# Kernel tuning notes

Hardware: AMD Instinct MI355X
Metric: run time of the kernel (lower is better)

## Reference

```python
import jax, jax.numpy as jnp
import numpy as np

NMS_RADIUS = 2.0   # cfgs.NMS_radius (meters)
EPS = 1e-6         # torch nn.PairwiseDistance default eps (added to the diff)
M = 16384          # number of keypoint candidates
SCENE = 100.0      # scene extent in meters


def setup_inputs() -> dict:
    key = jax.random.key(0)
    k1, k2 = jax.random.split(key)
    nodes = jax.random.uniform(k1, (M, 3), dtype=jnp.float32) * SCENE
    overlap_score = jax.random.normal(k2, (M,), dtype=jnp.float32)
    return {"nodes": nodes, "overlap_score": overlap_score}


def _greedy_nms(nodes, radius):
    """Sequential greedy NMS: keep node i iff its distance to every
    already-kept node exceeds radius. Faithful to the torch loop:
    (dis > radius).sum() == n_kept  <=>  all kept dists > radius."""
    n = nodes.shape[0]

    def body(i, mask):
        # torch nn.PairwiseDistance computes ||x1 - x2 + eps||_2
        d = jnp.linalg.norm(nodes[i] - nodes + EPS, axis=-1)  # [n]
        keep = jnp.all(jnp.where(mask, d > radius, True))
        return mask.at[i].set(keep)

    mask0 = jnp.zeros(n, dtype=bool).at[0].set(True)
    return jax.lax.fori_loop(1, n, body, mask0)


def reference(nodes, overlap_score):
    # sort by overlap score descending, run greedy NMS, unsort the mask
    order = jnp.argsort(-overlap_score)
    mask_sorted = _greedy_nms(nodes[order], NMS_RADIUS)
    mask = jnp.zeros_like(mask_sorted).at[order].set(mask_sorted)
    nms_length = mask.sum(dtype=jnp.int32)[None]
    return mask, nms_length
```

## Files before the change

kernel.cpp:

```cpp
#include <hip/hip_runtime.h>


#define M_PTS    16384
#define RADIUS   2.0f
#define EPS_D    1e-6f
#define GRID_N   25
#define NCELLS   (GRID_N * GRID_N * GRID_N)
#define CELL_CAP 12
#define K_NBR    12
#define ACT_CAP  4608


__device__ __forceinline__ int cell_of(float v) {
  int c = (int)(v * 0.25f);
  return c < 0 ? 0 : (c > GRID_N - 1 ? GRID_N - 1 : c);
}

__global__ __launch_bounds__(256) void zero_kernel(int4* __restrict__ p) {
  int i = blockIdx.x * 256 + threadIdx.x;
  if (i < 8003) p[i] = make_int4(0, 0, 0, 0);
}

__global__ __launch_bounds__(256) void grid_build(
    const float* __restrict__ nodes, const float* __restrict__ score,
    float4* __restrict__ pts, int* __restrict__ cell_cnt,
    unsigned short* __restrict__ cell_list) {
  int i = blockIdx.x * 256 + threadIdx.x;
  if (i >= M_PTS) return;
  float4 p;
  p.x = nodes[3 * i + 0];
  p.y = nodes[3 * i + 1];
  p.z = nodes[3 * i + 2];
  p.w = score[i];
  pts[i] = p;
  int cid = (cell_of(p.x) * GRID_N + cell_of(p.y)) * GRID_N + cell_of(p.z);
  int pos = atomicAdd(&cell_cnt[cid], 1);
  if (pos < CELL_CAP) cell_list[cid * CELL_CAP + pos] = (unsigned short)i;
}

__global__ __launch_bounds__(256) void nbr_scan(
    const float4* __restrict__ pts, const int* __restrict__ cell_cnt,
    const unsigned short* __restrict__ cell_list,
    int* __restrict__ cnt, unsigned short* __restrict__ nbr) {
  int t = blockIdx.x * 256 + threadIdx.x;
  int i = t / 27;
  int d = t - i * 27;
  if (i >= M_PTS) return;
  const float4 pi = pts[i];
  int cx = cell_of(pi.x) + (d / 9) - 1;
  int cy = cell_of(pi.y) + ((d / 3) % 3) - 1;
  int cz = cell_of(pi.z) + (d % 3) - 1;
  if (cx < 0 || cx >= GRID_N || cy < 0 || cy >= GRID_N ||
      cz < 0 || cz >= GRID_N) return;
  int cid = (cx * GRID_N + cy) * GRID_N + cz;
  int m = cell_cnt[cid];
  if (m > CELL_CAP) m = CELL_CAP;
  for (int s = 0; s < m; ++s) {
    int j = cell_list[cid * CELL_CAP + s];
    float4 pj = pts[j];
    bool earlier = (pj.w > pi.w) || ((pj.w == pi.w) && (j < i));
    if (!earlier) continue;
    float ddx = __fadd_rn(__fsub_rn(pi.x, pj.x), EPS_D);
    float ddy = __fadd_rn(__fsub_rn(pi.y, pj.y), EPS_D);
    float ddz = __fadd_rn(__fsub_rn(pi.z, pj.z), EPS_D);
    float d2 = __fadd_rn(__fadd_rn(__fmul_rn(ddx, ddx), __fmul_rn(ddy, ddy)),
                         __fmul_rn(ddz, ddz));
    float dist = __fsqrt_rn(d2);
    if (!(dist > RADIUS)) {
      int pos = atomicAdd(&cnt[i], 1);
      if (pos < K_NBR) nbr[i * K_NBR + pos] = (unsigned short)j;
    }
  }
}

__global__ __launch_bounds__(1024) void solve_kernel(
    const int* __restrict__ cnt, const unsigned short* __restrict__ nbr,
    int* __restrict__ out, int out_size) {
  __shared__ unsigned char mask_[M_PTS];
  __shared__ unsigned int nbr_s[ACT_CAP][6];
  __shared__ unsigned int act[ACT_CAP];
  __shared__ int act_n, total;
  volatile unsigned char* mask = mask_;

  const int tid = threadIdx.x;
  if (tid == 0) { act_n = 0; total = 0; }
  __syncthreads();

  for (int k = tid; k < M_PTS; k += 1024) {
    mask_[k] = 1;
    int c = cnt[k];
    if (c > K_NBR) c = K_NBR;
    if (c > 0) {
      int pos = atomicAdd(&act_n, 1);
      if (pos < ACT_CAP) act[pos] = (unsigned)k | ((unsigned)c << 16);
    }
  }
  __syncthreads();
  const int na_raw = act_n;
  const bool ok = (na_raw <= ACT_CAP);
  const int na = ok ? na_raw : ACT_CAP;

  if (ok) {
    for (int a = tid; a < na; a += 1024) {
      int k = (int)(act[a] & 0xFFFFu);
      const unsigned int* src = (const unsigned int*)(nbr + (size_t)k * K_NBR);
#pragma unroll
      for (int w = 0; w < 6; ++w) nbr_s[a][w] = src[w];
    }
  }
  __syncthreads();

  if (ok) {
    for (int grp = 0; grp < 128; ++grp) {
      for (int g = 0; g < 4; ++g) {
        for (int a = tid; a < na; a += 1024) {
          unsigned e = act[a];
          int k = (int)(e & 0xFFFFu);
          int c = (int)(e >> 16);
          const unsigned short* row = (const unsigned short*)nbr_s[a];
          int kp = 1;
          for (int t = 0; t < c; ++t) kp &= (int)(mask[row[t]] ^ 1);
          if (kp != (int)mask[k]) mask[k] = (unsigned char)kp;
        }
        asm volatile("" ::: "memory");
      }
      int any = 0;
      for (int a = tid; a < na; a += 1024) {
        unsigned e = act[a];
        int k = (int)(e & 0xFFFFu);
        int c = (int)(e >> 16);
        const unsigned short* row = (const unsigned short*)nbr_s[a];
        int kp = 1;
        for (int t = 0; t < c; ++t) kp &= (int)(mask[row[t]] ^ 1);
        if (kp != (int)mask[k]) { mask[k] = (unsigned char)kp; any = 1; }
      }
      if (__syncthreads_count(any) == 0) break;
    }
  } else {
    __shared__ int changed;
    for (int it = 0; it < 512; ++it) {
      if (tid == 0) changed = 0;
      __syncthreads();
      int any = 0;
      for (int k = tid; k < M_PTS; k += 1024) {
        int c = cnt[k]; if (c > K_NBR) c = K_NBR;
        if (!c) continue;
        int kp = 1;
        for (int t = 0; t < c; ++t) kp &= (int)(mask[nbr[k * K_NBR + t]] ^ 1);
        if (kp != (int)mask[k]) { mask_[k] = (unsigned char)kp; any = 1; }
      }
      if (any) changed = 1;
      __syncthreads();
      if (!changed) break;
    }
  }
  __syncthreads();

  int ks = 0;
  for (int k = tid; k < M_PTS; k += 1024) {
    int m = (int)mask_[k];
    out[k] = m;
    ks += m;
  }
#pragma unroll
  for (int off = 32; off > 0; off >>= 1) ks += __shfl_down(ks, off, 64);
  if ((tid & 63) == 0) atomicAdd(&total, ks);
  __syncthreads();
  if (tid == 0) out[out_size - 1] = total;
}

extern "C" void kernel_launch(void* const* d_in, const int* in_sizes, int n_in,
                              void* d_out, int out_size, void* d_ws, size_t ws_size,
                              hipStream_t stream) {
  const float* nodes = (const float*)d_in[0];
  const float* score = (const float*)d_in[1];
  int* out = (int*)d_out;

  char* ws = (char*)d_ws;
  float4* pts = (float4*)ws;
  int* cell_cnt = (int*)(ws + 262144);
  int* cnt = (int*)(ws + 324644);
  unsigned short* cell_list = (unsigned short*)(ws + 393216);
  unsigned short* nbr = (unsigned short*)(ws + 770048);

  zero_kernel<<<32, 256, 0, stream>>>((int4*)(ws + 262144));
  grid_build<<<64, 256, 0, stream>>>(nodes, score, pts, cell_cnt, cell_list);
  nbr_scan<<<1728, 256, 0, stream>>>(pts, cell_cnt, cell_list, cnt, nbr);
  solve_kernel<<<1, 1024, 0, stream>>>(cnt, nbr, out, out_size);
}
```

Baseline: 40.88 us.

## Keep active-point neighbor lists in registers and aggregate compaction atomics per wavefront

The solve kernel drops the shared-memory neighbor table. Each thread now holds up to five active entries, with their first three neighbor indices cached in registers, and falls back to global memory for longer lists. Compaction of active points uses one ballot-based atomic per wavefront instead of one per thread. The relaxation loop no longer runs four unsynchronized sweeps per check; it syncs after every sweep and is capped at 96 iterations, which may need more barriers and may stop before convergence if more passes are needed.

```diff
diff --git a/kernel.cpp b/kernel.cpp
--- a/kernel.cpp
+++ b/kernel.cpp
@@ -8,7 +8,8 @@
 #define NCELLS   (GRID_N * GRID_N * GRID_N)
 #define CELL_CAP 12
 #define K_NBR    12
-#define ACT_CAP  4608
+#define EPT      5
+#define ACT_PAD  (EPT * 1024)
 
 
 __device__ __forceinline__ int cell_of(float v) {
@@ -77,61 +78,68 @@
     const int* __restrict__ cnt, const unsigned short* __restrict__ nbr,
     int* __restrict__ out, int out_size) {
   __shared__ unsigned char mask_[M_PTS];
-  __shared__ unsigned int nbr_s[ACT_CAP][6];
-  __shared__ unsigned int act[ACT_CAP];
+  __shared__ unsigned int act[ACT_PAD];
   __shared__ int act_n, total;
   volatile unsigned char* mask = mask_;
 
   const int tid = threadIdx.x;
+  const int lane = tid & 63;
   if (tid == 0) { act_n = 0; total = 0; }
+  for (int a = tid; a < ACT_PAD; a += 1024) act[a] = 0u;
   __syncthreads();
 
   for (int k = tid; k < M_PTS; k += 1024) {
     mask_[k] = 1;
     int c = cnt[k];
     if (c > K_NBR) c = K_NBR;
+    unsigned long long b = __ballot(c > 0);
+    int wcnt = __popcll(b);
+    int wbase = 0;
+    if (lane == 0 && wcnt) wbase = atomicAdd(&act_n, wcnt);
+    wbase = __shfl(wbase, 0, 64);
     if (c > 0) {
-      int pos = atomicAdd(&act_n, 1);
-      if (pos < ACT_CAP) act[pos] = (unsigned)k | ((unsigned)c << 16);
+      int pos = wbase + __popcll(b & ((1ull << lane) - 1ull));
+      if (pos < ACT_PAD) act[pos] = (unsigned)k | ((unsigned)c << 16);
     }
   }
   __syncthreads();
-  const int na_raw = act_n;
-  const bool ok = (na_raw <= ACT_CAP);
-  const int na = ok ? na_raw : ACT_CAP;
+  const int na = act_n;
+  const bool ok = (na <= ACT_PAD);
 
-  if (ok) {
-    for (int a = tid; a < na; a += 1024) {
-      int k = (int)(act[a] & 0xFFFFu);
-      const unsigned int* src = (const unsigned int*)(nbr + (size_t)k * K_NBR);
+  unsigned ae[EPT];
+  unsigned short r0[EPT], r1[EPT], r2[EPT];
 #pragma unroll
-      for (int w = 0; w < 6; ++w) nbr_s[a][w] = src[w];
-    }
+  for (int e = 0; e < EPT; ++e) {
+    unsigned v = act[tid + e * 1024];
+    ae[e] = v;
+    int k = (int)(v & 0xFFFFu);
+    int c = (int)(v >> 16);
+    const unsigned short* row = nbr + (size_t)k * K_NBR;
+    r0[e] = (c > 0) ? row[0] : (unsigned short)0;
+    r1[e] = (c > 1) ? row[1] : (unsigned short)0;
+    r2[e] = (c > 2) ? row[2] : (unsigned short)0;
   }
   __syncthreads();
 
   if (ok) {
-    for (int grp = 0; grp < 128; ++grp) {
-      for (int g = 0; g < 4; ++g) {
-        for (int a = tid; a < na; a += 1024) {
-          unsigned e = act[a];
-          int k = (int)(e & 0xFFFFu);
-          int c = (int)(e >> 16);
-          const unsigned short* row = (const unsigned short*)nbr_s[a];
-          int kp = 1;
-          for (int t = 0; t < c; ++t) kp &= (int)(mask[row[t]] ^ 1);
-          if (kp != (int)mask[k]) mask[k] = (unsigned char)kp;
+    for (int it = 0; it < 96; ++it) {
+      int any = 0;
+      int m0[EPT];
+#pragma unroll
+      for (int e = 0; e < EPT; ++e) m0[e] = (int)mask[r0[e]];
+#pragma unroll
+      for (int e = 0; e < EPT; ++e) {
+        unsigned v = ae[e];
+        int c = (int)(v >> 16);
+        if (!c) continue;
+        int k = (int)(v & 0xFFFFu);
+        int kp = m0[e] ^ 1;
+        if (c > 1) kp &= (int)mask[r1[e]] ^ 1;
+        if (c > 2) kp &= (int)mask[r2[e]] ^ 1;
+        if (c > 3) {
+          const unsigned short* row = nbr + (size_t)k * K_NBR;
+          for (int t = 3; t < c; ++t) kp &= (int)mask[row[t]] ^ 1;
         }
-        asm volatile("" ::: "memory");
-      }
-      int any = 0;
-      for (int a = tid; a < na; a += 1024) {
-        unsigned e = act[a];
-        int k = (int)(e & 0xFFFFu);
-        int c = (int)(e >> 16);
-        const unsigned short* row = (const unsigned short*)nbr_s[a];
-        int kp = 1;
-        for (int t = 0; t < c; ++t) kp &= (int)(mask[row[t]] ^ 1);
         if (kp != (int)mask[k]) { mask[k] = (unsigned char)kp; any = 1; }
       }
       if (__syncthreads_count(any) == 0) break;
@@ -146,7 +154,7 @@
         int c = cnt[k]; if (c > K_NBR) c = K_NBR;
         if (!c) continue;
         int kp = 1;
-        for (int t = 0; t < c; ++t) kp &= (int)(mask[nbr[k * K_NBR + t]] ^ 1);
+        for (int t = 0; t < c; ++t) kp &= (int)mask[nbr[k * K_NBR + t]] ^ 1;
         if (kp != (int)mask[k]) { mask_[k] = (unsigned char)kp; any = 1; }
       }
       if (any) changed = 1;
@@ -164,7 +172,7 @@
   }
 #pragma unroll
   for (int off = 32; off > 0; off >>= 1) ks += __shfl_down(ks, off, 64);
-  if ((tid & 63) == 0) atomicAdd(&total, ks);
+  if (lane == 0) atomicAdd(&total, ks);
   __syncthreads();
   if (tid == 0) out[out_size - 1] = total;
 }
```

Result: no change. 40.57 us (-0.7%).
